# Kernel optimization log

Hardware: AMD Instinct MI355X
Metric: run time of the kernel (lower is better)

Reference implementation:

```python
import jax, jax.numpy as jnp
import numpy as np

B, T, D = 16, 4096, 64
K = 4096              # num_embeddings
DECAY = 0.99
COMMITMENT = 0.25
EPS = 1e-5


def setup_inputs() -> dict:
    key = jax.random.key(0)
    k1, k2 = jax.random.split(key)
    inputs = jax.random.normal(k1, (B, T, D), dtype=jnp.float32)
    # torch init: uniform_(-1/K, 1/K); _ema_w initialized to a copy of weight
    weight = jax.random.uniform(k2, (K, D), dtype=jnp.float32, minval=-1.0 / K, maxval=1.0 / K)
    return {
        "inputs": inputs,
        "weight": weight,
        "ema_cluster_size": jnp.zeros((K,), jnp.float32),
        "ema_w": weight,
    }


def reference(inputs, weight, ema_cluster_size, ema_w):
    b, t, d = inputs.shape
    flat = inputs.reshape(-1, d)                                   # [N, D]
    dist = (jnp.sum(flat * flat, axis=1, keepdims=True)
            + jnp.sum(weight * weight, axis=1)
            - 2.0 * flat @ weight.T)
    idx = jnp.argmin(dist, axis=1)                                 # [N]
    quantized = weight[idx].reshape(inputs.shape)                  # gather [B,T,D]

    # --- EMA codebook update (torch.no_grad path; one-hot matmuls == segment sums) ---
    counts = jax.ops.segment_sum(jnp.ones((flat.shape[0],), flat.dtype), idx, num_segments=K)
    cs = ema_cluster_size * DECAY + (1.0 - DECAY) * counts
    n = jnp.sum(cs)
    cs = (cs + EPS) / (n + K * EPS) * n                            # Laplace smoothing
    dw = jax.ops.segment_sum(flat, idx, num_segments=K)            # encodings.T @ flat
    new_ema_w = ema_w * DECAY + (1.0 - DECAY) * dw
    new_weight = new_ema_w / cs[:, None]

    # --- losses (on pre-update codebook, as in torch) ---
    e_latent = jnp.mean((jax.lax.stop_gradient(quantized) - inputs) ** 2)
    q_latent = jnp.mean((quantized - jax.lax.stop_gradient(inputs)) ** 2)
    loss = q_latent + COMMITMENT * e_latent

    # straight-through estimator
    quantized_st = inputs + jax.lax.stop_gradient(quantized - inputs)
    encoding_indices = idx.reshape(b, t)
    return quantized_st, loss, encoding_indices, new_weight, cs, new_ema_w
```

## Files before the change

kernel.cpp:

```cpp
#include <hip/hip_runtime.h>
#include <math.h>

#define NROWS 65536
#define DDIM  64
#define KCODE 4096
#define NSPLIT 4
#define KSPL  (KCODE / NSPLIT)
#define STEPS (KSPL / 16)

#define O_Q    0
#define O_LOSS 4194304
#define O_IDX  4194305
#define O_NW   4259841
#define O_CS   4521985
#define O_NEW  4526081

#define O_A      262144
#define O_B2     327680
#define O_CNT   1000000
#define O_OFF   1010000
#define O_CUR   1020000
#define O_ORD   1030000
#define O_LP64  1100000

typedef _Float16 f16x8 __attribute__((ext_vector_type(8)));
typedef float    f32x4 __attribute__((ext_vector_type(4)));

__global__ __launch_bounds__(256)
void vq_prep(const float* __restrict__ x, const float* __restrict__ w,
             float* __restrict__ out, unsigned long long* __restrict__ keys) {
    int i = blockIdx.x * 256 + threadIdx.x;
    {
        const int k = i >> 6, j = i & 63;
        float E = w[i] * 4096.0f;
        _Float16 h = (_Float16)E;
        float r = E - (float)h;
        _Float16 lo = (_Float16)(r * 4096.0f);
        const size_t pos = (size_t)(k >> 4) * 2048 + (size_t)(j >> 5) * 512
                         + (size_t)((j >> 3) & 3) * 128 + (size_t)(k & 15) * 8
                         + (size_t)(j & 7);
        ((_Float16*)out)[pos] = h;
        ((_Float16*)out)[pos + 1024] = lo;
    }
    if (i < NROWS) keys[i] = 0xFFFFFFFFFFFFFFFFULL;
    if (i < KCODE) ((unsigned*)(out + O_CNT))[i] = 0u;
    if ((i & 3) == 0) {
        const int row = i >> 2;
        const float4* xr = (const float4*)(x + (size_t)row * DDIM);
        float ax = 0.f, ay = 0.f, az = 0.f, aw = 0.f;
        #pragma unroll
        for (int j = 0; j < 16; ++j) {
            float4 v = xr[j];
            ax += v.x * v.x; ay += v.y * v.y; az += v.z * v.z; aw += v.w * v.w;
        }
        out[O_A + row] = (ax + ay) + (az + aw);
    }
    if ((i & 63) == 0) {
        const int k = i >> 6;
        const float4* wr = (const float4*)(w + (size_t)k * DDIM);
        float ax = 0.f, ay = 0.f, az = 0.f, aw = 0.f;
        #pragma unroll
        for (int j = 0; j < 16; ++j) {
            float4 v = wr[j];
            ax += v.x * v.x; ay += v.y * v.y; az += v.z * v.z; aw += v.w * v.w;
        }
        out[O_B2 + k] = (ax + ay) + (az + aw);
    }
}

__device__ inline void split8(float4 a, float4 b, f16x8& hi, f16x8& lo) {
    float vv[8] = {a.x, a.y, a.z, a.w, b.x, b.y, b.z, b.w};
    #pragma unroll
    for (int j = 0; j < 8; ++j) {
        float X = vv[j] * 256.0f;
        _Float16 h = (_Float16)X;
        float r = X - (float)h;
        hi[j] = h;
        lo[j] = (_Float16)(r * 4096.0f);
    }
}

__global__ __launch_bounds__(256, 2)
void vq_argmin_mfma(const float* __restrict__ x,
                    const _Float16* __restrict__ etab,
                    const float* __restrict__ Ag,
                    const float* __restrict__ b2g,
                    unsigned long long* __restrict__ keys) {
    __shared__ __align__(16) float b2sh[KSPL + 128];
    const int tid = threadIdx.x;
    const int k0  = blockIdx.y * KSPL;
    ((float4*)b2sh)[tid] = ((const float4*)(b2g + k0))[tid];
    __syncthreads();

    const int l   = tid & 63;
    const int w   = tid >> 6;
    const int g   = l >> 4;
    const int c16 = l & 15;
    const int rowbase = blockIdx.x * 256 + w * 64;

    f16x8 xh[4][2], xl[4][2];
    #pragma unroll
    for (int r = 0; r < 4; ++r) {
        const float* xr = x + (size_t)(rowbase + r * 16 + c16) * DDIM + g * 8;
        float4 a0 = *(const float4*)(xr);
        float4 a1 = *(const float4*)(xr + 4);
        float4 a2 = *(const float4*)(xr + 32);
        float4 a3 = *(const float4*)(xr + 36);
        split8(a0, a1, xh[r][0], xl[r][0]);
        split8(a2, a3, xh[r][1], xl[r][1]);
    }
    float A_reg[4][4];
    #pragma unroll
    for (int r = 0; r < 4; ++r)
        #pragma unroll
        for (int v = 0; v < 4; ++v)
            A_reg[r][v] = Ag[rowbase + r * 16 + 4 * g + v];

    float bestv[4][4]; int bidx[4][4];
    #pragma unroll
    for (int r = 0; r < 4; ++r)
        #pragma unroll
        for (int v = 0; v < 4; ++v) { bestv[r][v] = INFINITY; bidx[r][v] = 0; }

    const _Float16* p[2];
    p[0] = etab + (size_t)(k0 >> 4) * 2048 + (size_t)l * 8;
    p[1] = p[0] + 2048;

    f16x8 bh0[2], bh1[2], bl0[2], bl1[2];
    float b2r[2];
    int b2i[2] = {c16, 16 + c16};
    int cbase = k0 + c16;
    const f32x4 fzero = {0.f, 0.f, 0.f, 0.f};

#define LOADB(sl) do {                                       \
        bh0[sl] = *(const f16x8*)(p[sl]);                    \
        bh1[sl] = *(const f16x8*)(p[sl] + 512);              \
        bl0[sl] = *(const f16x8*)(p[sl] + 1024);             \
        bl1[sl] = *(const f16x8*)(p[sl] + 1536);             \
        b2r[sl] = b2sh[b2i[sl]];                             \
        p[sl] += 4096;                                       \
        b2i[sl] += 32;                                       \
    } while (0)

#define COMP(sl) do {                                                             \
        _Pragma("unroll")                                                         \
        for (int r = 0; r < 4; ++r) {                                             \
            f32x4 acc1, acc2;                                                     \
            acc1 = __builtin_amdgcn_mfma_f32_16x16x32_f16(xh[r][0], bh0[sl], fzero, 0, 0, 0); \
            acc1 = __builtin_amdgcn_mfma_f32_16x16x32_f16(xh[r][1], bh1[sl], acc1,  0, 0, 0); \
            acc2 = __builtin_amdgcn_mfma_f32_16x16x32_f16(xl[r][0], bh0[sl], fzero, 0, 0, 0); \
            acc2 = __builtin_amdgcn_mfma_f32_16x16x32_f16(xl[r][1], bh1[sl], acc2,  0, 0, 0); \
            acc2 = __builtin_amdgcn_mfma_f32_16x16x32_f16(xh[r][0], bl0[sl], acc2,  0, 0, 0); \
            acc2 = __builtin_amdgcn_mfma_f32_16x16x32_f16(xh[r][1], bl1[sl], acc2,  0, 0, 0); \
            _Pragma("unroll")                                                     \
            for (int v = 0; v < 4; ++v) {                                         \
                float dotc = fmaf(acc2[v], 0x1p-12f, acc1[v]);                    \
                float t = A_reg[r][v] + b2r[sl];                                  \
                float sc = fmaf(dotc, -0x1p-19f, t);                              \
                bool lt = sc < bestv[r][v];      \
                bestv[r][v] = lt ? sc : bestv[r][v];                              \
                bidx[r][v]  = lt ? cbase : bidx[r][v];                            \
            }                                                                     \
        }                                                                         \
        cbase += 16;                                                              \
    } while (0)

    LOADB(0);
    LOADB(1);

    #pragma unroll 1
    for (int s = 0; s < STEPS; s += 2) {
        COMP(0);
        LOADB(0);
        COMP(1);
        LOADB(1);
    }
#undef LOADB
#undef COMP

    #pragma unroll
    for (int off2 = 1; off2 < 16; off2 <<= 1) {
        #pragma unroll
        for (int r = 0; r < 4; ++r)
            #pragma unroll
            for (int v = 0; v < 4; ++v) {
                float ob = __shfl_xor(bestv[r][v], off2);
                int   oi = __shfl_xor(bidx[r][v], off2);
                if (ob < bestv[r][v] || (ob == bestv[r][v] && oi < bidx[r][v])) {
                    bestv[r][v] = ob; bidx[r][v] = oi;
                }
            }
    }
    if (c16 == 0) {
        #pragma unroll
        for (int r = 0; r < 4; ++r)
            #pragma unroll
            for (int v = 0; v < 4; ++v) {
                const int row = rowbase + r * 16 + 4 * g + v;
                unsigned long long key =
                    ((unsigned long long)__float_as_uint(bestv[r][v]) << 32) |
                    (unsigned)bidx[r][v];
                atomicMin(&keys[row], key);
            }
    }
}

__global__ __launch_bounds__(1024)
void vq_hist(const unsigned long long* __restrict__ keys,
             unsigned* __restrict__ counts, double* __restrict__ lp64) {
    __shared__ unsigned h[KCODE];
    __shared__ double dsh[16];
    const int tid = threadIdx.x;
    #pragma unroll
    for (int j = 0; j < 4; ++j) h[tid + j * 1024] = 0u;
    __syncthreads();
    const int row = blockIdx.x * 1024 + tid;
    const unsigned long long kk = keys[row];
    const unsigned k = (unsigned)(kk & 0xFFFFFFFFu);
    float sc = __uint_as_float((unsigned)(kk >> 32));
    atomicAdd(&h[k], 1u);
    #pragma unroll
    for (int off = 32; off > 0; off >>= 1) sc += __shfl_down(sc, off);
    if ((tid & 63) == 0) dsh[tid >> 6] = (double)sc;
    __syncthreads();
    if (tid == 0) {
        double s = 0.0;
        #pragma unroll
        for (int i = 0; i < 16; ++i) s += dsh[i];
        lp64[blockIdx.x] = s;
    }
    #pragma unroll
    for (int j = 0; j < 4; ++j) {
        unsigned v = h[tid + j * 1024];
        if (v) atomicAdd(&counts[tid + j * 1024], v);
    }
}

__global__ __launch_bounds__(1024)
void vq_scan_cs(const unsigned* __restrict__ counts, const float* __restrict__ ecs,
                const double* __restrict__ lp64,
                unsigned* __restrict__ offs, unsigned* __restrict__ cursor,
                float* __restrict__ out) {
    __shared__ unsigned red[1024];
    __shared__ float fred[1024];
    const int tid = threadIdx.x;
    unsigned c[4]; float csv[4];
    unsigned tot = 0; float fl = 0.f;
    #pragma unroll
    for (int j = 0; j < 4; ++j) {
        const int k = tid * 4 + j;
        c[j] = counts[k];
        tot += c[j];
        csv[j] = ecs[k] * 0.99f + 0.01f * (float)c[j];
        fl += csv[j];
    }
    red[tid] = tot; fred[tid] = fl;
    __syncthreads();
    for (int s = 1; s < 1024; s <<= 1) {
        unsigned v = (tid >= s) ? red[tid - s] : 0u;
        float  fv = (tid >= s) ? fred[tid - s] : 0.f;
        __syncthreads();
        red[tid] += v; fred[tid] += fv;
        __syncthreads();
    }
    const float n = fred[1023];
    unsigned base = red[tid] - tot;
    const float denom = n + 0.04096f;
    #pragma unroll
    for (int j = 0; j < 4; ++j) {
        const int k = tid * 4 + j;
        offs[k] = base; cursor[k] = base; base += c[j];
        out[O_CS + k] = (csv[j] + 1e-5f) / denom * n;
    }
    if (tid == 0) {
        double dl = 0.0;
        for (int i = 0; i < 64; ++i) dl += lp64[i];
        out[O_LOSS] = 1.25f * (float)(dl / 4194304.0);
    }
}

__global__ __launch_bounds__(256)
void vq_scatter(const unsigned long long* __restrict__ keys,
                unsigned* __restrict__ cursor, unsigned* __restrict__ order) {
    const int row = blockIdx.x * 256 + threadIdx.x;
    const unsigned k = (unsigned)(keys[row] & 0xFFFFFFFFu);
    const unsigned slot = atomicAdd(&cursor[k], 1u);
    order[slot] = row;
}

__global__ __launch_bounds__(256)
void vq_dw(const float* __restrict__ x, const float* __restrict__ ema_w,
           const unsigned* __restrict__ counts, const unsigned* __restrict__ offs,
           const unsigned* __restrict__ order, float* __restrict__ out) {
    const int tid = threadIdx.x;
    const int lane = tid & 63;
    const int k = blockIdx.x * 4 + (tid >> 6);
    const unsigned cnt = counts[k];
    const unsigned off = offs[k];
    float acc = 0.f;
    for (unsigned i = 0; i < cnt; ++i) {
        const unsigned row = order[off + i];
        acc += x[(size_t)row * DDIM + lane];
    }
    const float e = ema_w[(size_t)k * DDIM + lane];
    out[O_NEW + (size_t)k * DDIM + lane] = fmaf(0.01f, acc, 0.99f * e);
}

__global__ __launch_bounds__(256)
void vq_gather2(const float* __restrict__ x, const float* __restrict__ w,
                const unsigned long long* __restrict__ keys,
                float* __restrict__ out) {
    const int tid = threadIdx.x;
    const int l16 = tid & 15;
    const int row = blockIdx.x * 16 + (tid >> 4);
    const int k = (int)(unsigned)(keys[row] & 0xFFFFFFFFu);
    if (l16 == 0) out[O_IDX + row] = (float)k;
    const float4 w4 = ((const float4*)(w + (size_t)k * DDIM))[l16];
    const float4 x4 = ((const float4*)(x + (size_t)row * DDIM))[l16];
    float4 o;
    o.x = x4.x + (w4.x - x4.x);
    o.y = x4.y + (w4.y - x4.y);
    o.z = x4.z + (w4.z - x4.z);
    o.w = x4.w + (w4.w - x4.w);
    ((float4*)(out + O_Q + (size_t)row * DDIM))[l16] = o;
}

__global__ __launch_bounds__(256)
void vq_final(float* __restrict__ out) {
    int i = blockIdx.x * 256 + threadIdx.x;
    if (i >= KCODE * DDIM) return;
    int k = i >> 6;
    out[O_NW + i] = out[O_NEW + i] / out[O_CS + k];
}

extern "C" void kernel_launch(void* const* d_in, const int* in_sizes, int n_in,
                              void* d_out, int out_size, void* d_ws, size_t ws_size,
                              hipStream_t stream) {
    (void)in_sizes; (void)n_in; (void)out_size; (void)d_ws; (void)ws_size;
    const float* x    = (const float*)d_in[0];
    const float* w    = (const float*)d_in[1];
    const float* ecs  = (const float*)d_in[2];
    const float* emaw = (const float*)d_in[3];
    float* out = (float*)d_out;

    const _Float16* etab = (const _Float16*)out;
    const float*    Ag   = out + O_A;
    unsigned long long* keys = (unsigned long long*)(out + O_NW + 1);
    unsigned* counts = (unsigned*)(out + O_CNT);
    unsigned* offs   = (unsigned*)(out + O_OFF);
    unsigned* cursor = (unsigned*)(out + O_CUR);
    unsigned* order  = (unsigned*)(out + O_ORD);
    double*   lp64   = (double*)(out + O_LP64);

    vq_prep       <<<1024, 256, 0, stream>>>(x, w, out, keys);
    vq_argmin_mfma<<<dim3(256, NSPLIT), 256, 0, stream>>>(x, etab, Ag,
                                                          out + O_B2, keys);
    vq_hist       <<<64, 1024, 0, stream>>>(keys, counts, lp64);
    vq_scan_cs    <<<1, 1024, 0, stream>>>(counts, ecs, lp64, offs, cursor, out);
    vq_scatter    <<<256, 256, 0, stream>>>(keys, cursor, order);
    vq_dw         <<<1024, 256, 0, stream>>>(x, emaw, counts, offs, order, out);
    vq_gather2    <<<4096, 256, 0, stream>>>(x, w, keys, out);
    vq_final      <<<1024, 256, 0, stream>>>(out);
}
```

Baseline: 185.4 us.

## Switch argmin distance GEMM to 32x32x16 MFMA with re-laid codebook tiles

Replaces the 16x16x32 MFMA tiling (64 rows per wave, 4 row groups) with 32x32x16 MFMA tiles (32 rows by 32 codes per wave), and changes the fp16 hi/lo codebook layout in the prep kernel to match the new B-operand fragment order. Each wave now handles fewer rows, so the grid doubles in x, and the shuffle reduction spans 32 lanes. The aim is a better MFMA throughput-to-issue ratio and fewer instructions per code. In exchange, each wave reloads codebook fragments over twice as many waves and holds 16-wide accumulators, which raises register pressure.

```diff
diff --git a/kernel.cpp b/kernel.cpp
--- a/kernel.cpp
+++ b/kernel.cpp
@@ -6,7 +6,7 @@
 #define KCODE 4096
 #define NSPLIT 4
 #define KSPL  (KCODE / NSPLIT)
-#define STEPS (KSPL / 16)
+#define STEPS32 (KSPL / 32)
 
 #define O_Q    0
 #define O_LOSS 4194304
@@ -23,8 +23,8 @@
 #define O_ORD   1030000
 #define O_LP64  1100000
 
-typedef _Float16 f16x8 __attribute__((ext_vector_type(8)));
-typedef float    f32x4 __attribute__((ext_vector_type(4)));
+typedef _Float16 f16x8  __attribute__((ext_vector_type(8)));
+typedef float    f32x16 __attribute__((ext_vector_type(16)));
 
 __global__ __launch_bounds__(256)
 void vq_prep(const float* __restrict__ x, const float* __restrict__ w,
@@ -36,11 +36,11 @@
         _Float16 h = (_Float16)E;
         float r = E - (float)h;
         _Float16 lo = (_Float16)(r * 4096.0f);
-        const size_t pos = (size_t)(k >> 4) * 2048 + (size_t)(j >> 5) * 512
-                         + (size_t)((j >> 3) & 3) * 128 + (size_t)(k & 15) * 8
+        const size_t pos = (size_t)(k >> 5) * 4096 + (size_t)(j >> 4) * 512
+                         + (size_t)((((j >> 3) & 1) << 5) | (k & 31)) * 8
                          + (size_t)(j & 7);
         ((_Float16*)out)[pos] = h;
-        ((_Float16*)out)[pos + 1024] = lo;
+        ((_Float16*)out)[pos + 2048] = lo;
     }
     if (i < NROWS) keys[i] = 0xFFFFFFFFFFFFFFFFULL;
     if (i < KCODE) ((unsigned*)(out + O_CNT))[i] = 0u;
@@ -94,82 +94,82 @@
 
     const int l   = tid & 63;
     const int w   = tid >> 6;
-    const int g   = l >> 4;
-    const int c16 = l & 15;
-    const int rowbase = blockIdx.x * 256 + w * 64;
-
-    f16x8 xh[4][2], xl[4][2];
-    #pragma unroll
-    for (int r = 0; r < 4; ++r) {
-        const float* xr = x + (size_t)(rowbase + r * 16 + c16) * DDIM + g * 8;
-        float4 a0 = *(const float4*)(xr);
-        float4 a1 = *(const float4*)(xr + 4);
-        float4 a2 = *(const float4*)(xr + 32);
-        float4 a3 = *(const float4*)(xr + 36);
-        split8(a0, a1, xh[r][0], xl[r][0]);
-        split8(a2, a3, xh[r][1], xl[r][1]);
-    }
-    float A_reg[4][4];
-    #pragma unroll
-    for (int r = 0; r < 4; ++r)
-        #pragma unroll
-        for (int v = 0; v < 4; ++v)
-            A_reg[r][v] = Ag[rowbase + r * 16 + 4 * g + v];
-
-    float bestv[4][4]; int bidx[4][4];
-    #pragma unroll
-    for (int r = 0; r < 4; ++r)
-        #pragma unroll
-        for (int v = 0; v < 4; ++v) { bestv[r][v] = INFINITY; bidx[r][v] = 0; }
+    const int c32 = l & 31;
+    const int hb  = l >> 5;
+    const int rowbase = blockIdx.x * 128 + w * 32;
+
+    f16x8 xh[4], xl[4];
+    {
+        const float* xr = x + (size_t)(rowbase + c32) * DDIM + hb * 8;
+        #pragma unroll
+        for (int ks = 0; ks < 4; ++ks) {
+            float4 a0 = *(const float4*)(xr + ks * 16);
+            float4 a1 = *(const float4*)(xr + ks * 16 + 4);
+            split8(a0, a1, xh[ks], xl[ks]);
+        }
+    }
+    float A_reg[16];
+    #pragma unroll
+    for (int v = 0; v < 16; ++v)
+        A_reg[v] = Ag[rowbase + (v & 3) + 8 * (v >> 2) + 4 * hb];
+
+    float bestv[16]; int bidx[16];
+    #pragma unroll
+    for (int v = 0; v < 16; ++v) { bestv[v] = INFINITY; bidx[v] = 0; }
 
     const _Float16* p[2];
-    p[0] = etab + (size_t)(k0 >> 4) * 2048 + (size_t)l * 8;
-    p[1] = p[0] + 2048;
-
-    f16x8 bh0[2], bh1[2], bl0[2], bl1[2];
+    p[0] = etab + (size_t)(k0 >> 5) * 4096 + (size_t)l * 8;
+    p[1] = p[0] + 4096;
+
+    f16x8 BH[2][4], BL[2][4];
     float b2r[2];
-    int b2i[2] = {c16, 16 + c16};
-    int cbase = k0 + c16;
-    const f32x4 fzero = {0.f, 0.f, 0.f, 0.f};
-
-#define LOADB(sl) do {                                       \
-        bh0[sl] = *(const f16x8*)(p[sl]);                    \
-        bh1[sl] = *(const f16x8*)(p[sl] + 512);              \
-        bl0[sl] = *(const f16x8*)(p[sl] + 1024);             \
-        bl1[sl] = *(const f16x8*)(p[sl] + 1536);             \
-        b2r[sl] = b2sh[b2i[sl]];                             \
-        p[sl] += 4096;                                       \
-        b2i[sl] += 32;                                       \
+    int b2i[2] = {c32, 32 + c32};
+    int cbase = k0 + c32;
+    const f32x16 fzero = {0.f,0.f,0.f,0.f,0.f,0.f,0.f,0.f,
+                          0.f,0.f,0.f,0.f,0.f,0.f,0.f,0.f};
+
+#define LOADB(sl) do {                                        \
+        _Pragma("unroll")                                     \
+        for (int ks = 0; ks < 4; ++ks) {                      \
+            BH[sl][ks] = *(const f16x8*)(p[sl] + ks * 512);   \
+            BL[sl][ks] = *(const f16x8*)(p[sl] + 2048 + ks * 512); \
+        }                                                     \
+        b2r[sl] = b2sh[b2i[sl]];                              \
+        p[sl] += 8192;                                        \
+        b2i[sl] += 64;                                        \
     } while (0)
 
 #define COMP(sl) do {                                                             \
+        f32x16 a1, a2;                                                            \
+        a1 = __builtin_amdgcn_mfma_f32_32x32x16_f16(xh[0], BH[sl][0], fzero, 0, 0, 0); \
+        a1 = __builtin_amdgcn_mfma_f32_32x32x16_f16(xh[1], BH[sl][1], a1,    0, 0, 0); \
+        a1 = __builtin_amdgcn_mfma_f32_32x32x16_f16(xh[2], BH[sl][2], a1,    0, 0, 0); \
+        a1 = __builtin_amdgcn_mfma_f32_32x32x16_f16(xh[3], BH[sl][3], a1,    0, 0, 0); \
+        a2 = __builtin_amdgcn_mfma_f32_32x32x16_f16(xl[0], BH[sl][0], fzero, 0, 0, 0); \
+        a2 = __builtin_amdgcn_mfma_f32_32x32x16_f16(xl[1], BH[sl][1], a2,    0, 0, 0); \
+        a2 = __builtin_amdgcn_mfma_f32_32x32x16_f16(xl[2], BH[sl][2], a2,    0, 0, 0); \
+        a2 = __builtin_amdgcn_mfma_f32_32x32x16_f16(xl[3], BH[sl][3], a2,    0, 0, 0); \
+        a2 = __builtin_amdgcn_mfma_f32_32x32x16_f16(xh[0], BL[sl][0], a2,    0, 0, 0); \
+        a2 = __builtin_amdgcn_mfma_f32_32x32x16_f16(xh[1], BL[sl][1], a2,    0, 0, 0); \
+        a2 = __builtin_amdgcn_mfma_f32_32x32x16_f16(xh[2], BL[sl][2], a2,    0, 0, 0); \
+        a2 = __builtin_amdgcn_mfma_f32_32x32x16_f16(xh[3], BL[sl][3], a2,    0, 0, 0); \
         _Pragma("unroll")                                                         \
-        for (int r = 0; r < 4; ++r) {                                             \
-            f32x4 acc1, acc2;                                                     \
-            acc1 = __builtin_amdgcn_mfma_f32_16x16x32_f16(xh[r][0], bh0[sl], fzero, 0, 0, 0); \
-            acc1 = __builtin_amdgcn_mfma_f32_16x16x32_f16(xh[r][1], bh1[sl], acc1,  0, 0, 0); \
-            acc2 = __builtin_amdgcn_mfma_f32_16x16x32_f16(xl[r][0], bh0[sl], fzero, 0, 0, 0); \
-            acc2 = __builtin_amdgcn_mfma_f32_16x16x32_f16(xl[r][1], bh1[sl], acc2,  0, 0, 0); \
-            acc2 = __builtin_amdgcn_mfma_f32_16x16x32_f16(xh[r][0], bl0[sl], acc2,  0, 0, 0); \
-            acc2 = __builtin_amdgcn_mfma_f32_16x16x32_f16(xh[r][1], bl1[sl], acc2,  0, 0, 0); \
-            _Pragma("unroll")                                                     \
-            for (int v = 0; v < 4; ++v) {                                         \
-                float dotc = fmaf(acc2[v], 0x1p-12f, acc1[v]);                    \
-                float t = A_reg[r][v] + b2r[sl];                                  \
-                float sc = fmaf(dotc, -0x1p-19f, t);                              \
-                bool lt = sc < bestv[r][v];      \
-                bestv[r][v] = lt ? sc : bestv[r][v];                              \
-                bidx[r][v]  = lt ? cbase : bidx[r][v];                            \
-            }                                                                     \
+        for (int v = 0; v < 16; ++v) {                                            \
+            float dotc = fmaf(a2[v], 0x1p-12f, a1[v]);                            \
+            float t = A_reg[v] + b2r[sl];                                         \
+            float sc = fmaf(dotc, -0x1p-19f, t);                                  \
+            bool lt = sc < bestv[v];             \
+            bestv[v] = lt ? sc : bestv[v];                                        \
+            bidx[v]  = lt ? cbase : bidx[v];                                      \
         }                                                                         \
-        cbase += 16;                                                              \
+        cbase += 32;                                                              \
     } while (0)
 
     LOADB(0);
     LOADB(1);
 
     #pragma unroll 1
-    for (int s = 0; s < STEPS; s += 2) {
+    for (int s = 0; s < STEPS32; s += 2) {
         COMP(0);
         LOADB(0);
         COMP(1);
@@ -179,29 +179,25 @@
 #undef COMP
 
     #pragma unroll
-    for (int off2 = 1; off2 < 16; off2 <<= 1) {
-        #pragma unroll
-        for (int r = 0; r < 4; ++r)
-            #pragma unroll
-            for (int v = 0; v < 4; ++v) {
-                float ob = __shfl_xor(bestv[r][v], off2);
-                int   oi = __shfl_xor(bidx[r][v], off2);
-                if (ob < bestv[r][v] || (ob == bestv[r][v] && oi < bidx[r][v])) {
-                    bestv[r][v] = ob; bidx[r][v] = oi;
-                }
+    for (int off2 = 1; off2 < 32; off2 <<= 1) {
+        #pragma unroll
+        for (int v = 0; v < 16; ++v) {
+            float ob = __shfl_xor(bestv[v], off2);
+            int   oi = __shfl_xor(bidx[v], off2);
+            if (ob < bestv[v] || (ob == bestv[v] && oi < bidx[v])) {
+                bestv[v] = ob; bidx[v] = oi;
             }
-    }
-    if (c16 == 0) {
-        #pragma unroll
-        for (int r = 0; r < 4; ++r)
-            #pragma unroll
-            for (int v = 0; v < 4; ++v) {
-                const int row = rowbase + r * 16 + 4 * g + v;
-                unsigned long long key =
-                    ((unsigned long long)__float_as_uint(bestv[r][v]) << 32) |
-                    (unsigned)bidx[r][v];
-                atomicMin(&keys[row], key);
-            }
+        }
+    }
+    if (c32 == 0) {
+        #pragma unroll
+        for (int v = 0; v < 16; ++v) {
+            const int row = rowbase + (v & 3) + 8 * (v >> 2) + 4 * hb;
+            unsigned long long key =
+                ((unsigned long long)__float_as_uint(bestv[v]) << 32) |
+                (unsigned)bidx[v];
+            atomicMin(&keys[row], key);
+        }
     }
 }
 
@@ -353,7 +349,7 @@
     double*   lp64   = (double*)(out + O_LP64);
 
     vq_prep       <<<1024, 256, 0, stream>>>(x, w, out, keys);
-    vq_argmin_mfma<<<dim3(256, NSPLIT), 256, 0, stream>>>(x, etab, Ag,
+    vq_argmin_mfma<<<dim3(512, NSPLIT), 256, 0, stream>>>(x, etab, Ag,
                                                           out + O_B2, keys);
     vq_hist       <<<64, 1024, 0, stream>>>(keys, counts, lp64);
     vq_scan_cs    <<<1, 1024, 0, stream>>>(counts, ecs, lp64, offs, cursor, out);
```

Result: slower. 220.5 us (+18.9%).
